# Optimization experiments

Hardware: AMD Instinct MI355X
Metric: run time of the kernel (lower is better)

Reference implementation:

```python
import jax, jax.numpy as jnp
import numpy as np

B, N, T, C, H, E = 4, 256, 36, 64, 4, 4096
D = C // H          # per-head dim
CH = 2 * C          # GAT hidden channels (embed_size * 2)


def _ln(x, g, b):
    mu = x.mean(-1, keepdims=True)
    v = ((x - mu) ** 2).mean(-1, keepdims=True)
    return (x - mu) / jnp.sqrt(v + 1e-5) * g + b


def _gat_conv(x, src, dst, W, a_s, a_d, b):
    # GATConv, heads=1, add_self_loops=False, negative_slope=0.2
    h = x @ W                                        # [N, F]
    e = jax.nn.leaky_relu((h * a_s).sum(-1)[src] + (h * a_d).sum(-1)[dst], 0.2)  # [E]
    m = jax.ops.segment_max(e, dst, num_segments=N)  # per-dst softmax (stable)
    w = jnp.exp(e - m[dst])
    s = jax.ops.segment_sum(w, dst, num_segments=N)
    alpha = w / (s[dst] + 1e-16)
    return jax.ops.segment_sum(h[src] * alpha[:, None], dst, num_segments=N) + b


def _forward(query, key, value, edge_attr, D_S, W_emb, b_emb, Wq, Wk, Wv, W_fc, b_fc,
             ln1_g, ln1_b, ln2_g, ln2_b, W_ff1, b_ff1, W_ff2, b_ff2,
             gat1_W, gat1_as, gat1_ad, gat1_b, gat2_W, gat2_as, gat2_ad, gat2_b,
             jk_W, jk_b, W_fs, b_fs, W_fg, b_fg, edge_index):
    src, dst = edge_index[0], edge_index[1]

    def gat(x):  # [N, C] -> [N, C]; 2-layer GAT with jk='max'
        h1 = jax.nn.relu(_gat_conv(x, src, dst, gat1_W, gat1_as, gat1_ad, gat1_b))
        h2 = jax.nn.relu(_gat_conv(h1, src, dst, gat2_W, gat2_as, gat2_ad, gat2_b))
        return jnp.maximum(h1, h2) @ jk_W + jk_b

    # GAT is applied to the ORIGINAL query (before D_S is added), once per timestep.
    xg = jax.vmap(jax.vmap(gat))(query.transpose(0, 2, 1, 3))  # [B, T, N, C]
    # source loop PREPENDS each timestep's output -> time axis is reversed
    X_G = xg[:, ::-1].transpose(0, 2, 1, 3)                    # [B, N, T, C]

    ds = (D_S @ W_emb + b_emb)[None, :, None, :]               # [1, N, 1, C]
    q = query + ds
    k = key + ds
    v = value + ds

    qh = q.reshape(B, N, T, H, D) @ Wq                         # per-head shared linear
    kh = k.reshape(B, N, T, H, D) @ Wk
    vh = v.reshape(B, N, T, H, D) @ Wv
    attn = jnp.einsum('bqthd,bkthd->bqkth', qh, kh)            # [B, N, N, T, H]
    # NOTE: source softmaxes over dim=1 (the QUERY axis), scaled by sqrt(embed_size)
    a = jax.nn.softmax(attn / jnp.sqrt(jnp.float32(C)), axis=1)
    o = jnp.einsum('bqkth,bkthd->bqthd', a, vh).reshape(B, N, T, C)
    o = o @ W_fc + b_fc

    M_s = _ln(o + q, ln1_g, ln1_b)                             # dropout p=0 (identity)
    ff = jax.nn.relu(M_s @ W_ff1 + b_ff1) @ W_ff2 + b_ff2
    U_s = _ln(ff + M_s, ln2_g, ln2_b)

    g = jax.nn.sigmoid(U_s @ W_fs + b_fs + X_G @ W_fg + b_fg)
    return g * U_s + (1.0 - g) * X_G


def setup_inputs():
    key = jax.random.key(0)
    ki = iter(jax.random.split(key, 64))

    def p(shape):
        fan = shape[0]
        return jax.random.normal(next(ki), shape, dtype=jnp.float32) / jnp.float32(float(np.sqrt(fan)))

    inp = {}
    inp['query'] = jax.random.normal(next(ki), (B, N, T, C), dtype=jnp.float32)
    inp['key'] = jax.random.normal(next(ki), (B, N, T, C), dtype=jnp.float32)
    inp['value'] = jax.random.normal(next(ki), (B, N, T, C), dtype=jnp.float32)
    inp['edge_attr'] = jax.random.normal(next(ki), (E,), dtype=jnp.float32)
    inp['D_S'] = jax.random.normal(next(ki), (N, N), dtype=jnp.float32)  # adj, learned param
    inp['W_emb'] = p((N, C)); inp['b_emb'] = jnp.zeros((C,), jnp.float32)
    inp['Wq'] = p((D, D)); inp['Wk'] = p((D, D)); inp['Wv'] = p((D, D))
    inp['W_fc'] = p((C, C)); inp['b_fc'] = jnp.zeros((C,), jnp.float32)
    inp['ln1_g'] = jnp.ones((C,), jnp.float32); inp['ln1_b'] = jnp.zeros((C,), jnp.float32)
    inp['ln2_g'] = jnp.ones((C,), jnp.float32); inp['ln2_b'] = jnp.zeros((C,), jnp.float32)
    inp['W_ff1'] = p((C, 4 * C)); inp['b_ff1'] = jnp.zeros((4 * C,), jnp.float32)
    inp['W_ff2'] = p((4 * C, C)); inp['b_ff2'] = jnp.zeros((C,), jnp.float32)
    inp['gat1_W'] = p((C, CH)); inp['gat1_as'] = p((CH,)); inp['gat1_ad'] = p((CH,)); inp['gat1_b'] = jnp.zeros((CH,), jnp.float32)
    inp['gat2_W'] = p((CH, CH)); inp['gat2_as'] = p((CH,)); inp['gat2_ad'] = p((CH,)); inp['gat2_b'] = jnp.zeros((CH,), jnp.float32)
    inp['jk_W'] = p((CH, C)); inp['jk_b'] = jnp.zeros((C,), jnp.float32)
    inp['W_fs'] = p((C, C)); inp['b_fs'] = jnp.zeros((C,), jnp.float32)
    inp['W_fg'] = p((C, C)); inp['b_fg'] = jnp.zeros((C,), jnp.float32)
    inp['edge_index'] = jax.random.randint(next(ki), (2, E), 0, N, dtype=jnp.int32)
    return inp


def reference(query, key, value, edge_attr, D_S, W_emb, b_emb, Wq, Wk, Wv, W_fc, b_fc,
              ln1_g, ln1_b, ln2_g, ln2_b, W_ff1, b_ff1, W_ff2, b_ff2,
              gat1_W, gat1_as, gat1_ad, gat1_b, gat2_W, gat2_as, gat2_ad, gat2_b,
              jk_W, jk_b, W_fs, b_fs, W_fg, b_fg, edge_index):
    return _forward(query, key, value, edge_attr, D_S, W_emb, b_emb, Wq, Wk, Wv, W_fc, b_fc,
                    ln1_g, ln1_b, ln2_g, ln2_b, W_ff1, b_ff1, W_ff2, b_ff2,
                    gat1_W, gat1_as, gat1_ad, gat1_b, gat2_W, gat2_as, gat2_ad, gat2_b,
                    jk_W, jk_b, W_fs, b_fs, W_fg, b_fg, edge_index)
```

## Files before the change

### kernel.cpp

```cpp
#include <hip/hip_runtime.h>

typedef unsigned short u16;
typedef unsigned int u32;

#define B_ 4
#define N_ 256
#define T_ 36
#define C_ 64
#define H_ 4
#define D_ 16
#define CH_ 128
#define E_ 4096
#define EQ_ 1408
#define G_ (B_*T_)
#define TOK_ (B_*N_*T_)

#define DS_OFF  0
#define XG_OFF  (DS_OFF + N_*C_)
#define HA_OFF  (XG_OFF + TOK_*C_)
#define HB_OFF  (HA_OFF + G_*N_*CH_/2)
#define HS_OFF  (HB_OFF + G_*N_*CH_/2)
#define HD_OFF  (HS_OFF + G_*N_)
#define INT_OFF (HD_OFF + G_*N_)
#define MS_OFF  (INT_OFF + 4608)

__device__ __forceinline__ float bf2f(u16 u){
  u32 x = ((u32)u) << 16;
  return __builtin_bit_cast(float, x);
}
__device__ __forceinline__ u16 f2bf(float f){
  u32 x = __builtin_bit_cast(u32, f);
  x += 0x7fffu + ((x >> 16) & 1u);
  return (u16)(x >> 16);
}
__device__ __forceinline__ void unpack8(uint4 u, float* f){
  f[0]=bf2f((u16)(u.x & 0xffffu)); f[1]=bf2f((u16)(u.x >> 16));
  f[2]=bf2f((u16)(u.y & 0xffffu)); f[3]=bf2f((u16)(u.y >> 16));
  f[4]=bf2f((u16)(u.z & 0xffffu)); f[5]=bf2f((u16)(u.z >> 16));
  f[6]=bf2f((u16)(u.w & 0xffffu)); f[7]=bf2f((u16)(u.w >> 16));
}
__device__ __forceinline__ uint4 pack8f(const float* f){
  uint4 u;
  u.x = (u32)f2bf(f[0]) | ((u32)f2bf(f[1]) << 16);
  u.y = (u32)f2bf(f[2]) | ((u32)f2bf(f[3]) << 16);
  u.z = (u32)f2bf(f[4]) | ((u32)f2bf(f[5]) << 16);
  u.w = (u32)f2bf(f[6]) | ((u32)f2bf(f[7]) << 16);
  return u;
}
__device__ __forceinline__ int rfl(int v){ return __builtin_amdgcn_readfirstlane(v); }

__device__ __forceinline__ void gq_from_bid(int bid, int& g, int& q){
  int xc = bid & 7, slot = bid >> 3;
  q = slot & 3;
  g = xc + ((slot >> 2) << 3);
}

#define SP_ 20
// ... 101 lines not shown
    S.c.cnt[tid] = 0;
    __syncthreads();
    for (int e = tid; e < E_; e += 256) atomicAdd(&S.c.cnt[S.c.dstL[e]], 1);
    __syncthreads();
    if (tid == 0){
      int run = 0;
      for (int i = 0; i < N_; i++){ S.c.base[i] = run; run += S.c.cnt[i]; }
      S.c.base[N_] = run;
    }
    __syncthreads();
    S.c.cnt[tid] = 0;
    __syncthreads();
    for (int e = tid; e < E_; e += 256){
      int d = S.c.dstL[e];
      int p = atomicAdd(&S.c.cnt[d], 1);
      S.c.tmp[S.c.base[d] + p] = e;
    }
    __syncthreads();
    {
      const int p0 = S.c.base[tid], p1 = S.c.base[tid] + S.c.cnt[tid];
      for (int i = p0 + 1; i < p1; i++){
        int v = S.c.tmp[i]; int j = i - 1;
        while (j >= p0 && S.c.tmp[j] > v){ S.c.tmp[j+1] = S.c.tmp[j]; j--; }
        S.c.tmp[j+1] = v;
      }
      for (int j = p0; j < p1; j++) srcs[j] = S.c.srcL[S.c.tmp[j]];
    }
    indptr[tid] = S.c.base[tid];
    if (tid == 0) indptr[N_] = S.c.base[N_];
  }
}

__global__ __launch_bounds__(256)
void k_agg1(const u16* __restrict__ hin, const float* __restrict__ hs_ws, const float* __restrict__ hd_ws,
            const int* __restrict__ indptr, const int* __restrict__ srcs,
            const float* __restrict__ bias, u16* __restrict__ hout)
{
  __shared__ int   srcs_l[EQ_];
  __shared__ float alpha_l[EQ_];
  __shared__ float hs_l[N_];
  const int bid = blockIdx.x;
  int g, q; gq_from_bid(bid, g, q);
  const int n0 = q * 64;
  const int tid = threadIdx.x;

  const int p00 = indptr[n0];
  const int pend = indptr[n0 + 64];
  const int cntE = pend - p00;
  for (int i = tid; i < cntE; i += 256) srcs_l[i] = srcs[p00 + i];
  hs_l[tid] = hs_ws[g*N_ + tid];
  __syncthreads();

  edge_softmax_par(tid, n0, indptr, p00, srcs_l, hs_l, hd_ws, g, alpha_l);
  __syncthreads();

  const int r = tid & 63;
  const int cb = rfl(tid >> 6);
  const int ch0 = cb * 32;
  const int dst = n0 + r;
  const int p0 = indptr[dst] - p00, p1 = indptr[dst+1] - p00;

  float acc[32];
  #pragma unroll
  for (int j = 0; j < 32; j++) acc[j] = 0.f;
  for (int j = p0; j < p1; j++){
    float a = alpha_l[j];
    int s = srcs_l[j];
    const uint4* hp = (const uint4*)(hin + ((size_t)(g*N_ + s))*CH_ + ch0);
    #pragma unroll
    for (int qq = 0; qq < 4; qq++){
      float hv[8]; unpack8(hp[qq], hv);
      #pragma unroll
      for (int i = 0; i < 8; i++) acc[qq*8+i] += a * hv[i];
    }
  }
  float o[32];
  #pragma unroll
  for (int j = 0; j < 32; j++){
    float v = acc[j] + bias[ch0+j];
    o[j] = v > 0.f ? v : 0.f;
  }
  u16* op = hout + ((size_t)(g*N_ + dst))*CH_ + ch0;
  #pragma unroll
  for (int j8 = 0; j8 < 32; j8 += 8)
    *(uint4*)(op + j8) = pack8f(&o[j8]);
}

__global__ __launch_bounds__(256)
void k_lin2(const u16* __restrict__ h1, const float* __restrict__ W2,
            const float* __restrict__ as2, const float* __restrict__ ad2,
            u16* __restrict__ h2, float* __restrict__ hs_ws, float* __restrict__ hd_ws)
{
  __shared__ float xs[64][129];
  __shared__ float red[2][4][64];
  const int bid = blockIdx.x;
  int g, q; gq_from_bid(bid, g, q);
  const int n0 = q * 64;
  const int tid = threadIdx.x;

  {
    #pragma unroll
    for (int it = 0; it < 4; it++){
      int idx = tid + 256*it;
      int row = idx >> 4, c8 = (idx & 15) * 8;
      uint4 u = *(const uint4*)(h1 + ((size_t)(g*N_ + n0 + row))*CH_ + c8);
      float v[8]; unpack8(u, v);
      #pragma unroll
      for (int i = 0; i < 8; i++) xs[row][c8+i] = v[i];
    }
  }
  __syncthreads();

  const int r = tid & 63;
  const int cb = rfl(tid >> 6);
  const int ch0 = cb * 32;

  float acc[32];
  #pragma unroll
  for (int j = 0; j < 32; j++) acc[j] = 0.f;
  for (int k = 0; k < 128; k++){
    float xv = xs[r][k];
    const float* wrow = W2 + k*CH_ + ch0;
    #pragma unroll
    for (int j = 0; j < 32; j++) acc[j] += xv * wrow[j];
  }
  float hs = 0.f, hd = 0.f;
  #pragma unroll
  for (int j = 0; j < 32; j++){ hs += acc[j]*as2[ch0+j]; hd += acc[j]*ad2[ch0+j]; }
  red[0][cb][r] = hs; red[1][cb][r] = hd;

  u16* hp = h2 + ((size_t)(g*N_ + n0 + r))*CH_ + ch0;
  #pragma unroll
  for (int j8 = 0; j8 < 32; j8 += 8)
    *(uint4*)(hp + j8) = pack8f(&acc[j8]);

  __syncthreads();
  if (tid < 64){
    float a = red[0][0][tid]+red[0][1][tid]+red[0][2][tid]+red[0][3][tid];
    float d = red[1][0][tid]+red[1][1][tid]+red[1][2][tid]+red[1][3][tid];
    hs_ws[g*N_ + n0 + tid] = a;
    hd_ws[g*N_ + n0 + tid] = d;
  }
}

__global__ __launch_bounds__(256)
void k_aggjk(const u16* __restrict__ h2, const float* __restrict__ hs_ws, const float* __restrict__ hd_ws,
             const int* __restrict__ indptr, const int* __restrict__ srcs,
             const float* __restrict__ b2, const u16* __restrict__ h1,
             const float* __restrict__ jkW, const float* __restrict__ jkb, float* __restrict__ xg,
             const float* __restrict__ query, const float* __restrict__ key,
             const float* __restrict__ Wq, const float* __restrict__ Wk,
             const float* __restrict__ dsb, float* __restrict__ mS)
{
  __shared__ union UJ {
    struct { int srcs_l[EQ_]; float alpha_l[EQ_]; float hs_l[N_]; } a;
    struct { u16 xs[64][136]; } l;
    struct { float qs[N_][SP_]; float wq[16][16]; float wk[16][16]; } s;
  } U;
  const int bid = blockIdx.x;
  const int tid = threadIdx.x;

  if (bid < 576){
    int g, q; gq_from_bid(bid, g, q);
    const int n0 = q * 64;
    const int b = g / T_, t = g % T_;

    const int p00 = indptr[n0];
    const int pend = indptr[n0 + 64];
    const int cntE = pend - p00;
    for (int i = tid; i < cntE; i += 256) U.a.srcs_l[i] = srcs[p00 + i];
    U.a.hs_l[tid] = hs_ws[g*N_ + tid];
    __syncthreads();

    edge_softmax_par(tid, n0, indptr, p00, U.a.srcs_l, U.a.hs_l, hd_ws, g, U.a.alpha_l);
    __syncthreads();

    const int r = tid & 63;
    const int cb = rfl(tid >> 6);
    const int ch0 = cb * 32;
    const int dst = n0 + r;
    const int p0 = indptr[dst] - p00, p1 = indptr[dst+1] - p00;

    float acc[32];
    #pragma unroll
    for (int j = 0; j < 32; j++) acc[j] = 0.f;
    for (int j = p0; j < p1; j++){
      float a = U.a.alpha_l[j];
      int s = U.a.srcs_l[j];
      const uint4* hp = (const uint4*)(h2 + ((size_t)(g*N_ + s))*CH_ + ch0);
      #pragma unroll
      for (int qq = 0; qq < 4; qq++){
        float hv[8]; unpack8(hp[qq], hv);
        #pragma unroll
        for (int i = 0; i < 8; i++) acc[qq*8+i] += a * hv[i];
      }
    }
    float o[32];
    {
      const uint4* h1p = (const uint4*)(h1 + ((size_t)(g*N_ + dst))*CH_ + ch0);
      #pragma unroll
      for (int j8 = 0; j8 < 32; j8 += 8){
        float h1v[8]; unpack8(h1p[j8>>3], h1v);
        #pragma unroll
        for (int i = 0; i < 8; i++){
          float v = acc[j8+i] + b2[ch0+j8+i];
          v = v > 0.f ? v : 0.f;
          o[j8+i] = fmaxf(h1v[i], v);
        }
      }
    }
    __syncthreads();

    #pragma unroll
    for (int j8 = 0; j8 < 32; j8 += 8)
      *(uint4*)&U.l.xs[r][ch0 + j8] = pack8f(&o[j8]);
    __syncthreads();

    const int o0 = cb * 16;
    float acc2[16];
    #pragma unroll
    for (int j = 0; j < 16; j++) acc2[j] = 0.f;
    for (int k8 = 0; k8 < 16; k8++){
      uint4 u = *(const uint4*)&U.l.xs[r][k8*8];
      float hv[8]; unpack8(u, hv);
      #pragma unroll
      for (int kk = 0; kk < 8; kk++){
        const float* wrow = jkW + (k8*8+kk)*C_ + o0;
        #pragma unroll
        for (int j = 0; j < 16; j++) acc2[j] += hv[kk] * wrow[j];
      }
    }
    float* op = xg + ((((size_t)b*N_ + n0 + r)*T_) + (T_-1-t))*C_ + o0;
    #pragma unroll
    for (int j4 = 0; j4 < 16; j4 += 4){
      float4 v = make_float4(acc2[j4]+jkb[o0+j4], acc2[j4+1]+jkb[o0+j4+1],
                             acc2[j4+2]+jkb[o0+j4+2], acc2[j4+3]+jkb[o0+j4+3]);
      *(float4*)(op + j4) = v;
    }
  } else {
    const int sb = bid - 576;
    const int b = sb / (T_*H_);
    const int rem = sb % (T_*H_);
    const int t = rem / H_;
    const int h = rem % H_;
    const int n = tid;

    U.s.wq[n>>4][n&15] = Wq[n];
    U.s.wk[n>>4][n&15] = Wk[n];

    const size_t base = ((((size_t)b*N_ + n)*T_) + t)*C_ + h*D_;
    const float* dsp = dsb + n*C_ + h*D_;

    float x[16];
    #pragma unroll
    for (int j4 = 0; j4 < 16; j4 += 4){
      float4 a = *(const float4*)(query + base + j4);
      float4 d = *(const float4*)(dsp + j4);
      x[j4]=a.x+d.x; x[j4+1]=a.y+d.y; x[j4+2]=a.z+d.z; x[j4+3]=a.w+d.w;
    }
    __syncthreads();
    #pragma unroll
    for (int j = 0; j < 16; j++){
      float a = 0.f;
      #pragma unroll
      for (int i = 0; i < 16; i++) a += x[i]*U.s.wq[i][j];
      U.s.qs[n][j] = a;
    }
    float khr[16];
    #pragma unroll
    for (int j4 = 0; j4 < 16; j4 += 4){
      float4 a = *(const float4*)(key + base + j4);
// ... 9 lines not shown
    }
    __syncthreads();

    float m[4], s[4];
    #pragma unroll
    for (int c = 0; c < 4; c++){ m[c] = -1e30f; s[c] = 0.f; }
    for (int qq = 0; qq < 64; qq++){
      #pragma unroll
      for (int c = 0; c < 4; c++){
        const float* qrow = &U.s.qs[qq + 64*c][0];
        float4 a0 = *(const float4*)(qrow);
        float4 a1 = *(const float4*)(qrow+4);
        float4 a2 = *(const float4*)(qrow+8);
        float4 a3 = *(const float4*)(qrow+12);
        float d = a0.x*khr[0]+a0.y*khr[1]+a0.z*khr[2]+a0.w*khr[3]
                + a1.x*khr[4]+a1.y*khr[5]+a1.z*khr[6]+a1.w*khr[7]
                + a2.x*khr[8]+a2.y*khr[9]+a2.z*khr[10]+a2.w*khr[11]
                + a3.x*khr[12]+a3.y*khr[13]+a3.z*khr[14]+a3.w*khr[15];
        d *= 0.125f;
        float mn = fmaxf(m[c], d);
        s[c] = s[c]*__expf(m[c]-mn) + __expf(d-mn);
        m[c] = mn;
      }
    }
    float M = fmaxf(fmaxf(m[0],m[1]), fmaxf(m[2],m[3]));
    float S = s[0]*__expf(m[0]-M) + s[1]*__expf(m[1]-M)
            + s[2]*__expf(m[2]-M) + s[3]*__expf(m[3]-M);
    mS[(size_t)sb*512 + n*2]     = M;
    mS[(size_t)sb*512 + n*2 + 1] = 1.f / S;
  }
}

__global__ __launch_bounds__(256)
void k_av(const float* __restrict__ query, const float* __restrict__ key, const float* __restrict__ value,
          const float* __restrict__ Wq, const float* __restrict__ Wk, const float* __restrict__ Wv,
          const float* __restrict__ dsb, const float* __restrict__ mS, float* __restrict__ o_ws)
{
  __shared__ float ks[N_][SP_];
  __shared__ float vs[N_][SP_];
  __shared__ float2 msl[N_];
  __shared__ float wq[16][16], wk[16][16], wv[16][16];

  const int bx = blockIdx.x;
  const int b = bx / (T_*H_);
  const int rem = bx % (T_*H_);
  const int t = rem / H_;
  const int h = rem % H_;
  const int n = threadIdx.x;

  wq[n>>4][n&15] = Wq[n];
  wk[n>>4][n&15] = Wk[n];
  wv[n>>4][n&15] = Wv[n];
  msl[n] = *(const float2*)(mS + (size_t)bx*512 + n*2);

  const size_t base = ((((size_t)b*N_ + n)*T_) + t)*C_ + h*D_;
  const float* dsp = dsb + n*C_ + h*D_;

  float ds16[16];
  #pragma unroll
  for (int j4 = 0; j4 < 16; j4 += 4){
    float4 d = *(const float4*)(dsp + j4);
    ds16[j4]=d.x; ds16[j4+1]=d.y; ds16[j4+2]=d.z; ds16[j4+3]=d.w;
  }
  __syncthreads();

  float x[16];
  #pragma unroll
  for (int j4 = 0; j4 < 16; j4 += 4){
    float4 a = *(const float4*)(key + base + j4);
    x[j4]=a.x+ds16[j4]; x[j4+1]=a.y+ds16[j4+1]; x[j4+2]=a.z+ds16[j4+2]; x[j4+3]=a.w+ds16[j4+3];
  }
  #pragma unroll
  for (int j = 0; j < 16; j++){
    float a = 0.f;
    #pragma unroll
    for (int i = 0; i < 16; i++) a += x[i]*wk[i][j];
    ks[n][j] = a;
  }
  #pragma unroll
  for (int j4 = 0; j4 < 16; j4 += 4){
    float4 a = *(const float4*)(value + base + j4);
    x[j4]=a.x+ds16[j4]; x[j4+1]=a.y+ds16[j4+1]; x[j4+2]=a.z+ds16[j4+2]; x[j4+3]=a.w+ds16[j4+3];
  }
  #pragma unroll
  for (int j = 0; j < 16; j++){
    float a = 0.f;
    #pragma unroll
    for (int i = 0; i < 16; i++) a += x[i]*wv[i][j];
    vs[n][j] = a;
  }
  float qhr[16];
  #pragma unroll
  for (int j4 = 0; j4 < 16; j4 += 4){
    float4 a = *(const float4*)(query + base + j4);
    x[j4]=a.x+ds16[j4]; x[j4+1]=a.y+ds16[j4+1]; x[j4+2]=a.z+ds16[j4+2]; x[j4+3]=a.w+ds16[j4+3];
  }
  #pragma unroll
  for (int j = 0; j < 16; j++){
    float a = 0.f;
    #pragma unroll
    for (int i = 0; i < 16; i++) a += x[i]*wq[i][j];
    qhr[j] = a;
  }
  __syncthreads();

  float o0[16], o1[16];
  #pragma unroll
  for (int j = 0; j < 16; j++){ o0[j] = 0.f; o1[j] = 0.f; }
  for (int k = 0; k < N_; k += 2){
    {
      const float* krow = &ks[k][0];
      float4 a0 = *(const float4*)(krow);
      float4 a1 = *(const float4*)(krow+4);
      float4 a2 = *(const float4*)(krow+8);
      float4 a3 = *(const float4*)(krow+12);
      float d = a0.x*qhr[0]+a0.y*qhr[1]+a0.z*qhr[2]+a0.w*qhr[3]
              + a1.x*qhr[4]+a1.y*qhr[5]+a1.z*qhr[6]+a1.w*qhr[7]
              + a2.x*qhr[8]+a2.y*qhr[9]+a2.z*qhr[10]+a2.w*qhr[11]
              + a3.x*qhr[12]+a3.y*qhr[13]+a3.z*qhr[14]+a3.w*qhr[15];
      float2 ms0 = msl[k];
      float p = __expf(d*0.125f - ms0.x) * ms0.y;
      const float* vrow = &vs[k][0];
      float4 v0 = *(const float4*)(vrow);
      float4 v1 = *(const float4*)(vrow+4);
      float4 v2 = *(const float4*)(vrow+8);
      float4 v3 = *(const float4*)(vrow+12);
      o0[0]+=p*v0.x; o0[1]+=p*v0.y; o0[2]+=p*v0.z; o0[3]+=p*v0.w;
      o0[4]+=p*v1.x; o0[5]+=p*v1.y; o0[6]+=p*v1.z; o0[7]+=p*v1.w;
      o0[8]+=p*v2.x; o0[9]+=p*v2.y; o0[10]+=p*v2.z; o0[11]+=p*v2.w;
      o0[12]+=p*v3.x; o0[13]+=p*v3.y; o0[14]+=p*v3.z; o0[15]+=p*v3.w;
    }
    {
      const float* krow = &ks[k+1][0];
      float4 a0 = *(const float4*)(krow);
      float4 a1 = *(const float4*)(krow+4);
      float4 a2 = *(const float4*)(krow+8);
      float4 a3 = *(const float4*)(krow+12);
      float d = a0.x*qhr[0]+a0.y*qhr[1]+a0.z*qhr[2]+a0.w*qhr[3]
              + a1.x*qhr[4]+a1.y*qhr[5]+a1.z*qhr[6]+a1.w*qhr[7]
              + a2.x*qhr[8]+a2.y*qhr[9]+a2.z*qhr[10]+a2.w*qhr[11]
              + a3.x*qhr[12]+a3.y*qhr[13]+a3.z*qhr[14]+a3.w*qhr[15];
      float2 ms1 = msl[k+1];
      float p = __expf(d*0.125f - ms1.x) * ms1.y;
      const float* vrow = &vs[k+1][0];
      float4 v0 = *(const float4*)(vrow);
      float4 v1 = *(const float4*)(vrow+4);
      float4 v2 = *(const float4*)(vrow+8);
      float4 v3 = *(const float4*)(vrow+12);
      o1[0]+=p*v0.x; o1[1]+=p*v0.y; o1[2]+=p*v0.z; o1[3]+=p*v0.w;
      o1[4]+=p*v1.x; o1[5]+=p*v1.y; o1[6]+=p*v1.z; o1[7]+=p*v1.w;
      o1[8]+=p*v2.x; o1[9]+=p*v2.y; o1[10]+=p*v2.z; o1[11]+=p*v2.w;
      o1[12]+=p*v3.x; o1[13]+=p*v3.y; o1[14]+=p*v3.z; o1[15]+=p*v3.w;
    }
  }
  float* op = o_ws + base;
  #pragma unroll
  for (int j4 = 0; j4 < 16; j4 += 4)
    *(float4*)(op + j4) = make_float4(o0[j4]+o1[j4], o0[j4+1]+o1[j4+1],
                                      o0[j4+2]+o1[j4+2], o0[j4+3]+o1[j4+3]);
}

__global__ __launch_bounds__(256)
void k_final(const float* __restrict__ query, const float* __restrict__ dsb,
             const float* __restrict__ o_ws, const float* __restrict__ xg_ws,
             const float* __restrict__ Wfc, const float* __restrict__ bfc,
             const float* __restrict__ ln1g, const float* __restrict__ ln1b,
             const float* __restrict__ ln2g, const float* __restrict__ ln2b,
             const float* __restrict__ Wff1, const float* __restrict__ bff1,
             const float* __restrict__ Wff2, const float* __restrict__ bff2,
             const float* __restrict__ Wfs, const float* __restrict__ bfs,
             const float* __restrict__ Wfg, const float* __restrict__ bfg,
             float* __restrict__ out)
{
  __shared__ u16 smA[64*66];
  __shared__ u16 smB[64*66];
  __shared__ union UH { u16 h[128*66]; float o[64*66]; } HH;
  __shared__ float lnxA[4][64];
  __shared__ float lnxB[4][64];

  const int tid = threadIdx.x;
  const int token0 = blockIdx.x * 64;
  const int w = rfl(tid >> 6);
  const int tok = tid & 63;
  const int c0 = w * 16;

  #pragma unroll
  for (int it = 0; it < 4; it++){
    int idx = tid + 256*it;
    int tk = idx >> 4, c4 = (idx & 15) * 4;
    int gtok = token0 + tk;
    int n = (gtok / T_) & (N_-1);
    float4 ov = *(const float4*)(o_ws + (size_t)gtok*C_ + c4);
// ... 118 lines not shown
    float xv = bf2f(HH.h[i*66 + tok]);
    const float* wsr = Wfs + i*C_ + c0;
    const float* wgr = Wfg + i*C_ + c0;
    #pragma unroll
    for (int j = 0; j < 16; j++) ga[j] += uv*wsr[j] + xv*wgr[j];
  }
  float res[16];
  #pragma unroll
  for (int j = 0; j < 16; j++){
    float a = ga[j] + bfs[c0+j] + bfg[c0+j];
    float gg = 1.f / (1.f + __expf(-a));
    float xgv = bf2f(HH.h[(c0+j)*66 + tok]);
    res[j] = gg*us[j] + (1.f-gg)*xgv;
  }
  __syncthreads();
  #pragma unroll
  for (int j = 0; j < 16; j++) HH.o[(c0+j)*66 + tok] = res[j];
  __syncthreads();
  #pragma unroll
  for (int it = 0; it < 4; it++){
    int idx = tid + 256*it;
    int tk = idx >> 4, c4 = (idx & 15) * 4;
    int gtok = token0 + tk;
    float4 v = make_float4(HH.o[(c4+0)*66+tk], HH.o[(c4+1)*66+tk],
                           HH.o[(c4+2)*66+tk], HH.o[(c4+3)*66+tk]);
    *(float4*)(out + (size_t)gtok*C_ + c4) = v;
  }
}

extern "C" void kernel_launch(void* const* d_in, const int* in_sizes, int n_in,
                              void* d_out, int out_size, void* d_ws, size_t ws_size,
                              hipStream_t stream)
{
  (void)in_sizes; (void)n_in; (void)out_size; (void)ws_size;
  const float* query = (const float*)d_in[0];
  const float* key   = (const float*)d_in[1];
  const float* value = (const float*)d_in[2];
  const float* DSm   = (const float*)d_in[4];
  const float* Wemb  = (const float*)d_in[5];
  const float* bemb  = (const float*)d_in[6];
  const float* Wq    = (const float*)d_in[7];
  const float* Wk    = (const float*)d_in[8];
  const float* Wv    = (const float*)d_in[9];
  const float* Wfc   = (const float*)d_in[10];
  const float* bfc   = (const float*)d_in[11];
  const float* ln1g  = (const float*)d_in[12];
  const float* ln1b  = (const float*)d_in[13];
  const float* ln2g  = (const float*)d_in[14];
  const float* ln2b  = (const float*)d_in[15];
  const float* Wff1  = (const float*)d_in[16];
  const float* bff1  = (const float*)d_in[17];
  const float* Wff2  = (const float*)d_in[18];
  const float* bff2  = (const float*)d_in[19];
  const float* g1W   = (const float*)d_in[20];
  const float* g1as  = (const float*)d_in[21];
  const float* g1ad  = (const float*)d_in[22];
  const float* g1b   = (const float*)d_in[23];
  const float* g2W   = (const float*)d_in[24];
  const float* g2as  = (const float*)d_in[25];
  const float* g2ad  = (const float*)d_in[26];
  const float* g2b   = (const float*)d_in[27];
  const float* jkW   = (const float*)d_in[28];
  const float* jkb   = (const float*)d_in[29];
  const float* Wfs   = (const float*)d_in[30];
  const float* bfs   = (const float*)d_in[31];
  const float* Wfg   = (const float*)d_in[32];
  const float* bfg   = (const float*)d_in[33];
  const int* ei      = (const int*)d_in[34];
  float* out = (float*)d_out;

  float* wf     = (float*)d_ws;
  float* dsb    = wf + DS_OFF;
  float* xg_ws  = wf + XG_OFF;
  u16*   hA     = (u16*)(wf + HA_OFF);
  u16*   hB     = (u16*)(wf + HB_OFF);
  float* o_ws   = wf + HA_OFF;
  float* hs_ws  = wf + HS_OFF;
  float* hd_ws  = wf + HD_OFF;
  int*   indptr = (int*)(wf + INT_OFF);
  int*   srcs   = indptr + 260;
  float* mS     = wf + MS_OFF;

  k_pre  <<<dim3(641),  dim3(256), 0, stream>>>(query, g1W, g1as, g1ad, hA, hs_ws, hd_ws,
                                                DSm, Wemb, bemb, dsb, ei, indptr, srcs);
  k_agg1 <<<dim3(576),  dim3(256), 0, stream>>>(hA, hs_ws, hd_ws, indptr, srcs, g1b, hB);
  k_lin2 <<<dim3(576),  dim3(256), 0, stream>>>(hB, g2W, g2as, g2ad, hA, hs_ws, hd_ws);
  k_aggjk<<<dim3(1152), dim3(256), 0, stream>>>(hA, hs_ws, hd_ws, indptr, srcs, g2b, hB,
                                                jkW, jkb, xg_ws,
                                                query, key, Wq, Wk, dsb, mS);
  k_av   <<<dim3(576),  dim3(256), 0, stream>>>(query, key, value, Wq, Wk, Wv, dsb, mS, o_ws);
  k_final<<<dim3(576),  dim3(256), 0, stream>>>(query, dsb, o_ws, xg_ws,
      Wfc, bfc, ln1g, ln1b, ln2g, ln2b,
      Wff1, bff1, Wff2, bff2,
      Wfs, bfs, Wfg, bfg, out);
}
```

Before: 304.6 us.

## Rebalance kernel pairing: attention stats with GAT layer 1, AV with GAT layer 2

The attention softmax-statistics blocks move from the layer-2 aggregation kernel into the layer-1 aggregation kernel. The attention AV blocks are merged into the layer-2 aggregation plus JK kernel, which removes one launch and lets independent work share the GPU. To run AV at the same time as aggregation, the AV output gets its own workspace region rather than aliasing the hA buffer. If the workspace is too small, the code falls back to two sequential launches. The cost is a larger shared-memory union and larger workspace use.

```diff
diff --git a/kernel.cpp b/kernel.cpp
--- a/kernel.cpp
+++ b/kernel.cpp
@@ -23,6 +23,7 @@
 #define HD_OFF  (HS_OFF + G_*N_)
 #define INT_OFF (HD_OFF + G_*N_)
 #define MS_OFF  (INT_OFF + 4608)
+#define O_SEP_OFF (MS_OFF + 576*512)
 
 __device__ __forceinline__ float bf2f(u16 u){
   u32 x = ((u32)u) << 16;
@@ -190,129 +191,15 @@
 }
 
 __global__ __launch_bounds__(256)
-void k_agg1(const u16* __restrict__ hin, const float* __restrict__ hs_ws, const float* __restrict__ hd_ws,
-            const int* __restrict__ indptr, const int* __restrict__ srcs,
-            const float* __restrict__ bias, u16* __restrict__ hout)
+void k_agg1stat(const u16* __restrict__ hin, const float* __restrict__ hs_ws, const float* __restrict__ hd_ws,
+                const int* __restrict__ indptr, const int* __restrict__ srcs,
+                const float* __restrict__ bias, u16* __restrict__ hout,
+                const float* __restrict__ query, const float* __restrict__ key,
+                const float* __restrict__ Wq, const float* __restrict__ Wk,
+                const float* __restrict__ dsb, float* __restrict__ mS)
 {
-  __shared__ int   srcs_l[EQ_];
-  __shared__ float alpha_l[EQ_];
-  __shared__ float hs_l[N_];
-  const int bid = blockIdx.x;
-  int g, q; gq_from_bid(bid, g, q);
-  const int n0 = q * 64;
-  const int tid = threadIdx.x;
-
-  const int p00 = indptr[n0];
-  const int pend = indptr[n0 + 64];
-  const int cntE = pend - p00;
-  for (int i = tid; i < cntE; i += 256) srcs_l[i] = srcs[p00 + i];
-  hs_l[tid] = hs_ws[g*N_ + tid];
-  __syncthreads();
-
-  edge_softmax_par(tid, n0, indptr, p00, srcs_l, hs_l, hd_ws, g, alpha_l);
-  __syncthreads();
-
-  const int r = tid & 63;
-  const int cb = rfl(tid >> 6);
-  const int ch0 = cb * 32;
-  const int dst = n0 + r;
-  const int p0 = indptr[dst] - p00, p1 = indptr[dst+1] - p00;
-
-  float acc[32];
-  #pragma unroll
-  for (int j = 0; j < 32; j++) acc[j] = 0.f;
-  for (int j = p0; j < p1; j++){
-    float a = alpha_l[j];
-    int s = srcs_l[j];
-    const uint4* hp = (const uint4*)(hin + ((size_t)(g*N_ + s))*CH_ + ch0);
-    #pragma unroll
-    for (int qq = 0; qq < 4; qq++){
-      float hv[8]; unpack8(hp[qq], hv);
-      #pragma unroll
-      for (int i = 0; i < 8; i++) acc[qq*8+i] += a * hv[i];
-    }
-  }
-  float o[32];
-  #pragma unroll
-  for (int j = 0; j < 32; j++){
-    float v = acc[j] + bias[ch0+j];
-    o[j] = v > 0.f ? v : 0.f;
-  }
-  u16* op = hout + ((size_t)(g*N_ + dst))*CH_ + ch0;
-  #pragma unroll
-  for (int j8 = 0; j8 < 32; j8 += 8)
-    *(uint4*)(op + j8) = pack8f(&o[j8]);
-}
-
-__global__ __launch_bounds__(256)
-void k_lin2(const u16* __restrict__ h1, const float* __restrict__ W2,
-            const float* __restrict__ as2, const float* __restrict__ ad2,
-            u16* __restrict__ h2, float* __restrict__ hs_ws, float* __restrict__ hd_ws)
-{
-  __shared__ float xs[64][129];
-  __shared__ float red[2][4][64];
-  const int bid = blockIdx.x;
-  int g, q; gq_from_bid(bid, g, q);
-  const int n0 = q * 64;
-  const int tid = threadIdx.x;
-
-  {
-    #pragma unroll
-    for (int it = 0; it < 4; it++){
-      int idx = tid + 256*it;
-      int row = idx >> 4, c8 = (idx & 15) * 8;
-      uint4 u = *(const uint4*)(h1 + ((size_t)(g*N_ + n0 + row))*CH_ + c8);
-      float v[8]; unpack8(u, v);
-      #pragma unroll
-      for (int i = 0; i < 8; i++) xs[row][c8+i] = v[i];
-    }
-  }
-  __syncthreads();
-
-  const int r = tid & 63;
-  const int cb = rfl(tid >> 6);
-  const int ch0 = cb * 32;
-
-  float acc[32];
-  #pragma unroll
-  for (int j = 0; j < 32; j++) acc[j] = 0.f;
-  for (int k = 0; k < 128; k++){
-    float xv = xs[r][k];
-    const float* wrow = W2 + k*CH_ + ch0;
-    #pragma unroll
-    for (int j = 0; j < 32; j++) acc[j] += xv * wrow[j];
-  }
-  float hs = 0.f, hd = 0.f;
-  #pragma unroll
-  for (int j = 0; j < 32; j++){ hs += acc[j]*as2[ch0+j]; hd += acc[j]*ad2[ch0+j]; }
-  red[0][cb][r] = hs; red[1][cb][r] = hd;
-
-  u16* hp = h2 + ((size_t)(g*N_ + n0 + r))*CH_ + ch0;
-  #pragma unroll
-  for (int j8 = 0; j8 < 32; j8 += 8)
-    *(uint4*)(hp + j8) = pack8f(&acc[j8]);
-
-  __syncthreads();
-  if (tid < 64){
-    float a = red[0][0][tid]+red[0][1][tid]+red[0][2][tid]+red[0][3][tid];
-    float d = red[1][0][tid]+red[1][1][tid]+red[1][2][tid]+red[1][3][tid];
-    hs_ws[g*N_ + n0 + tid] = a;
-    hd_ws[g*N_ + n0 + tid] = d;
-  }
-}
-
-__global__ __launch_bounds__(256)
-void k_aggjk(const u16* __restrict__ h2, const float* __restrict__ hs_ws, const float* __restrict__ hd_ws,
-             const int* __restrict__ indptr, const int* __restrict__ srcs,
-             const float* __restrict__ b2, const u16* __restrict__ h1,
-             const float* __restrict__ jkW, const float* __restrict__ jkb, float* __restrict__ xg,
-             const float* __restrict__ query, const float* __restrict__ key,
-             const float* __restrict__ Wq, const float* __restrict__ Wk,
-             const float* __restrict__ dsb, float* __restrict__ mS)
-{
-  __shared__ union UJ {
+  __shared__ union UA {
     struct { int srcs_l[EQ_]; float alpha_l[EQ_]; float hs_l[N_]; } a;
-    struct { u16 xs[64][136]; } l;
     struct { float qs[N_][SP_]; float wq[16][16]; float wk[16][16]; } s;
   } U;
   const int bid = blockIdx.x;
@@ -321,7 +208,6 @@
   if (bid < 576){
     int g, q; gq_from_bid(bid, g, q);
     const int n0 = q * 64;
-    const int b = g / T_, t = g % T_;
 
     const int p00 = indptr[n0];
     const int pend = indptr[n0 + 64];
@@ -345,7 +231,7 @@
     for (int j = p0; j < p1; j++){
       float a = U.a.alpha_l[j];
       int s = U.a.srcs_l[j];
-      const uint4* hp = (const uint4*)(h2 + ((size_t)(g*N_ + s))*CH_ + ch0);
+      const uint4* hp = (const uint4*)(hin + ((size_t)(g*N_ + s))*CH_ + ch0);
       #pragma unroll
       for (int qq = 0; qq < 4; qq++){
         float hv[8]; unpack8(hp[qq], hv);
@@ -354,47 +240,15 @@
       }
     }
     float o[32];
-    {
-      const uint4* h1p = (const uint4*)(h1 + ((size_t)(g*N_ + dst))*CH_ + ch0);
-      #pragma unroll
-      for (int j8 = 0; j8 < 32; j8 += 8){
-        float h1v[8]; unpack8(h1p[j8>>3], h1v);
-        #pragma unroll
-        for (int i = 0; i < 8; i++){
-          float v = acc[j8+i] + b2[ch0+j8+i];
-          v = v > 0.f ? v : 0.f;
-          o[j8+i] = fmaxf(h1v[i], v);
-        }
-      }
-    }
-    __syncthreads();
-
+    #pragma unroll
+    for (int j = 0; j < 32; j++){
+      float v = acc[j] + bias[ch0+j];
+      o[j] = v > 0.f ? v : 0.f;
+    }
+    u16* op = hout + ((size_t)(g*N_ + dst))*CH_ + ch0;
     #pragma unroll
     for (int j8 = 0; j8 < 32; j8 += 8)
-      *(uint4*)&U.l.xs[r][ch0 + j8] = pack8f(&o[j8]);
-    __syncthreads();
-
-    const int o0 = cb * 16;
-    float acc2[16];
-    #pragma unroll
-    for (int j = 0; j < 16; j++) acc2[j] = 0.f;
-    for (int k8 = 0; k8 < 16; k8++){
-      uint4 u = *(const uint4*)&U.l.xs[r][k8*8];
-      float hv[8]; unpack8(u, hv);
-      #pragma unroll
-      for (int kk = 0; kk < 8; kk++){
-        const float* wrow = jkW + (k8*8+kk)*C_ + o0;
-        #pragma unroll
-        for (int j = 0; j < 16; j++) acc2[j] += hv[kk] * wrow[j];
-      }
-    }
-    float* op = xg + ((((size_t)b*N_ + n0 + r)*T_) + (T_-1-t))*C_ + o0;
-    #pragma unroll
-    for (int j4 = 0; j4 < 16; j4 += 4){
-      float4 v = make_float4(acc2[j4]+jkb[o0+j4], acc2[j4+1]+jkb[o0+j4+1],
-                             acc2[j4+2]+jkb[o0+j4+2], acc2[j4+3]+jkb[o0+j4+3]);
-      *(float4*)(op + j4) = v;
-    }
+      *(uint4*)(op + j8) = pack8f(&o[j8]);
   } else {
     const int sb = bid - 576;
     const int b = sb / (T_*H_);
@@ -470,132 +324,277 @@
 }
 
 __global__ __launch_bounds__(256)
-void k_av(const float* __restrict__ query, const float* __restrict__ key, const float* __restrict__ value,
-          const float* __restrict__ Wq, const float* __restrict__ Wk, const float* __restrict__ Wv,
-          const float* __restrict__ dsb, const float* __restrict__ mS, float* __restrict__ o_ws)
+void k_lin2(const u16* __restrict__ h1, const float* __restrict__ W2,
+            const float* __restrict__ as2, const float* __restrict__ ad2,
+            u16* __restrict__ h2, float* __restrict__ hs_ws, float* __restrict__ hd_ws)
 {
-  __shared__ float ks[N_][SP_];
-  __shared__ float vs[N_][SP_];
-  __shared__ float2 msl[N_];
-  __shared__ float wq[16][16], wk[16][16], wv[16][16];
-
-  const int bx = blockIdx.x;
-  const int b = bx / (T_*H_);
-  const int rem = bx % (T_*H_);
-  const int t = rem / H_;
-  const int h = rem % H_;
-  const int n = threadIdx.x;
-
-  wq[n>>4][n&15] = Wq[n];
-  wk[n>>4][n&15] = Wk[n];
-  wv[n>>4][n&15] = Wv[n];
-  msl[n] = *(const float2*)(mS + (size_t)bx*512 + n*2);
-
-  const size_t base = ((((size_t)b*N_ + n)*T_) + t)*C_ + h*D_;
-  const float* dsp = dsb + n*C_ + h*D_;
-
-  float ds16[16];
-  #pragma unroll
-  for (int j4 = 0; j4 < 16; j4 += 4){
-    float4 d = *(const float4*)(dsp + j4);
-    ds16[j4]=d.x; ds16[j4+1]=d.y; ds16[j4+2]=d.z; ds16[j4+3]=d.w;
-  }
-  __syncthreads();
-
-  float x[16];
-  #pragma unroll
-  for (int j4 = 0; j4 < 16; j4 += 4){
-    float4 a = *(const float4*)(key + base + j4);
-    x[j4]=a.x+ds16[j4]; x[j4+1]=a.y+ds16[j4+1]; x[j4+2]=a.z+ds16[j4+2]; x[j4+3]=a.w+ds16[j4+3];
-  }
-  #pragma unroll
-  for (int j = 0; j < 16; j++){
-    float a = 0.f;
-    #pragma unroll
-    for (int i = 0; i < 16; i++) a += x[i]*wk[i][j];
-    ks[n][j] = a;
-  }
-  #pragma unroll
-  for (int j4 = 0; j4 < 16; j4 += 4){
-    float4 a = *(const float4*)(value + base + j4);
-    x[j4]=a.x+ds16[j4]; x[j4+1]=a.y+ds16[j4+1]; x[j4+2]=a.z+ds16[j4+2]; x[j4+3]=a.w+ds16[j4+3];
-  }
-  #pragma unroll
-  for (int j = 0; j < 16; j++){
-    float a = 0.f;
-    #pragma unroll
-    for (int i = 0; i < 16; i++) a += x[i]*wv[i][j];
-    vs[n][j] = a;
-  }
-  float qhr[16];
-  #pragma unroll
-  for (int j4 = 0; j4 < 16; j4 += 4){
-    float4 a = *(const float4*)(query + base + j4);
-    x[j4]=a.x+ds16[j4]; x[j4+1]=a.y+ds16[j4+1]; x[j4+2]=a.z+ds16[j4+2]; x[j4+3]=a.w+ds16[j4+3];
-  }
-  #pragma unroll
-  for (int j = 0; j < 16; j++){
-    float a = 0.f;
-    #pragma unroll
-    for (int i = 0; i < 16; i++) a += x[i]*wq[i][j];
-    qhr[j] = a;
-  }
-  __syncthreads();
-
-  float o0[16], o1[16];
-  #pragma unroll
-  for (int j = 0; j < 16; j++){ o0[j] = 0.f; o1[j] = 0.f; }
-  for (int k = 0; k < N_; k += 2){
+  __shared__ float xs[64][129];
+  __shared__ float red[2][4][64];
+  const int bid = blockIdx.x;
+  int g, q; gq_from_bid(bid, g, q);
+  const int n0 = q * 64;
+  const int tid = threadIdx.x;
+
+  {
+    #pragma unroll
+    for (int it = 0; it < 4; it++){
+      int idx = tid + 256*it;
+      int row = idx >> 4, c8 = (idx & 15) * 8;
+      uint4 u = *(const uint4*)(h1 + ((size_t)(g*N_ + n0 + row))*CH_ + c8);
+      float v[8]; unpack8(u, v);
+      #pragma unroll
+      for (int i = 0; i < 8; i++) xs[row][c8+i] = v[i];
+    }
+  }
+  __syncthreads();
+
+  const int r = tid & 63;
+  const int cb = rfl(tid >> 6);
+  const int ch0 = cb * 32;
+
+  float acc[32];
+  #pragma unroll
+  for (int j = 0; j < 32; j++) acc[j] = 0.f;
+  for (int k = 0; k < 128; k++){
+    float xv = xs[r][k];
+    const float* wrow = W2 + k*CH_ + ch0;
+    #pragma unroll
+    for (int j = 0; j < 32; j++) acc[j] += xv * wrow[j];
+  }
+  float hs = 0.f, hd = 0.f;
+  #pragma unroll
+  for (int j = 0; j < 32; j++){ hs += acc[j]*as2[ch0+j]; hd += acc[j]*ad2[ch0+j]; }
+  red[0][cb][r] = hs; red[1][cb][r] = hd;
+
+  u16* hp = h2 + ((size_t)(g*N_ + n0 + r))*CH_ + ch0;
+  #pragma unroll
+  for (int j8 = 0; j8 < 32; j8 += 8)
+    *(uint4*)(hp + j8) = pack8f(&acc[j8]);
+
+  __syncthreads();
+  if (tid < 64){
+    float a = red[0][0][tid]+red[0][1][tid]+red[0][2][tid]+red[0][3][tid];
+    float d = red[1][0][tid]+red[1][1][tid]+red[1][2][tid]+red[1][3][tid];
+    hs_ws[g*N_ + n0 + tid] = a;
+    hd_ws[g*N_ + n0 + tid] = d;
+  }
+}
+
+__global__ __launch_bounds__(256)
+void k_agg2av(const u16* __restrict__ h2, const float* __restrict__ hs_ws, const float* __restrict__ hd_ws,
+              const int* __restrict__ indptr, const int* __restrict__ srcs,
+              const float* __restrict__ b2, const u16* __restrict__ h1,
+              const float* __restrict__ jkW, const float* __restrict__ jkb, float* __restrict__ xg,
+              const float* __restrict__ query, const float* __restrict__ key, const float* __restrict__ value,
+              const float* __restrict__ Wq, const float* __restrict__ Wk, const float* __restrict__ Wv,
+              const float* __restrict__ dsb, const float* __restrict__ mS, float* __restrict__ o_ws,
+              int bid_base)
+{
+  __shared__ union UJ {
+    struct { int srcs_l[EQ_]; float alpha_l[EQ_]; float hs_l[N_]; } a;
+    struct { u16 xs[64][136]; } l;
+    struct { float ks[N_][SP_]; float vs[N_][SP_]; float2 msl[N_];
+             float wq[16][16]; float wk[16][16]; float wv[16][16]; } v;
+  } U;
+  const int bid = blockIdx.x + bid_base;
+  const int tid = threadIdx.x;
+
+  if (bid < 576){
+    int g, q; gq_from_bid(bid, g, q);
+    const int n0 = q * 64;
+    const int b = g / T_, t = g % T_;
+
+    const int p00 = indptr[n0];
+    const int pend = indptr[n0 + 64];
+    const int cntE = pend - p00;
+    for (int i = tid; i < cntE; i += 256) U.a.srcs_l[i] = srcs[p00 + i];
+    U.a.hs_l[tid] = hs_ws[g*N_ + tid];
+    __syncthreads();
+
+    edge_softmax_par(tid, n0, indptr, p00, U.a.srcs_l, U.a.hs_l, hd_ws, g, U.a.alpha_l);
+    __syncthreads();
+
+    const int r = tid & 63;
+    const int cb = rfl(tid >> 6);
+    const int ch0 = cb * 32;
+    const int dst = n0 + r;
+    const int p0 = indptr[dst] - p00, p1 = indptr[dst+1] - p00;
+
+    float acc[32];
+    #pragma unroll
+    for (int j = 0; j < 32; j++) acc[j] = 0.f;
+    for (int j = p0; j < p1; j++){
+      float a = U.a.alpha_l[j];
+      int s = U.a.srcs_l[j];
+      const uint4* hp = (const uint4*)(h2 + ((size_t)(g*N_ + s))*CH_ + ch0);
+      #pragma unroll
+      for (int qq = 0; qq < 4; qq++){
+        float hv[8]; unpack8(hp[qq], hv);
+        #pragma unroll
+        for (int i = 0; i < 8; i++) acc[qq*8+i] += a * hv[i];
+      }
+    }
+    float o[32];
     {
-      const float* krow = &ks[k][0];
-      float4 a0 = *(const float4*)(krow);
-      float4 a1 = *(const float4*)(krow+4);
-      float4 a2 = *(const float4*)(krow+8);
-      float4 a3 = *(const float4*)(krow+12);
-      float d = a0.x*qhr[0]+a0.y*qhr[1]+a0.z*qhr[2]+a0.w*qhr[3]
-              + a1.x*qhr[4]+a1.y*qhr[5]+a1.z*qhr[6]+a1.w*qhr[7]
-              + a2.x*qhr[8]+a2.y*qhr[9]+a2.z*qhr[10]+a2.w*qhr[11]
-              + a3.x*qhr[12]+a3.y*qhr[13]+a3.z*qhr[14]+a3.w*qhr[15];
-      float2 ms0 = msl[k];
-      float p = __expf(d*0.125f - ms0.x) * ms0.y;
-      const float* vrow = &vs[k][0];
-      float4 v0 = *(const float4*)(vrow);
-      float4 v1 = *(const float4*)(vrow+4);
-      float4 v2 = *(const float4*)(vrow+8);
-      float4 v3 = *(const float4*)(vrow+12);
-      o0[0]+=p*v0.x; o0[1]+=p*v0.y; o0[2]+=p*v0.z; o0[3]+=p*v0.w;
-      o0[4]+=p*v1.x; o0[5]+=p*v1.y; o0[6]+=p*v1.z; o0[7]+=p*v1.w;
-      o0[8]+=p*v2.x; o0[9]+=p*v2.y; o0[10]+=p*v2.z; o0[11]+=p*v2.w;
-      o0[12]+=p*v3.x; o0[13]+=p*v3.y; o0[14]+=p*v3.z; o0[15]+=p*v3.w;
-    }
-    {
-      const float* krow = &ks[k+1][0];
-      float4 a0 = *(const float4*)(krow);
-      float4 a1 = *(const float4*)(krow+4);
-      float4 a2 = *(const float4*)(krow+8);
-      float4 a3 = *(const float4*)(krow+12);
-      float d = a0.x*qhr[0]+a0.y*qhr[1]+a0.z*qhr[2]+a0.w*qhr[3]
-              + a1.x*qhr[4]+a1.y*qhr[5]+a1.z*qhr[6]+a1.w*qhr[7]
-              + a2.x*qhr[8]+a2.y*qhr[9]+a2.z*qhr[10]+a2.w*qhr[11]
-              + a3.x*qhr[12]+a3.y*qhr[13]+a3.z*qhr[14]+a3.w*qhr[15];
-      float2 ms1 = msl[k+1];
-      float p = __expf(d*0.125f - ms1.x) * ms1.y;
-      const float* vrow = &vs[k+1][0];
-      float4 v0 = *(const float4*)(vrow);
-      float4 v1 = *(const float4*)(vrow+4);
-      float4 v2 = *(const float4*)(vrow+8);
-      float4 v3 = *(const float4*)(vrow+12);
-      o1[0]+=p*v0.x; o1[1]+=p*v0.y; o1[2]+=p*v0.z; o1[3]+=p*v0.w;
-      o1[4]+=p*v1.x; o1[5]+=p*v1.y; o1[6]+=p*v1.z; o1[7]+=p*v1.w;
-      o1[8]+=p*v2.x; o1[9]+=p*v2.y; o1[10]+=p*v2.z; o1[11]+=p*v2.w;
-      o1[12]+=p*v3.x; o1[13]+=p*v3.y; o1[14]+=p*v3.z; o1[15]+=p*v3.w;
-    }
-  }
-  float* op = o_ws + base;
-  #pragma unroll
-  for (int j4 = 0; j4 < 16; j4 += 4)
-    *(float4*)(op + j4) = make_float4(o0[j4]+o1[j4], o0[j4+1]+o1[j4+1],
-                                      o0[j4+2]+o1[j4+2], o0[j4+3]+o1[j4+3]);
+      const uint4* h1p = (const uint4*)(h1 + ((size_t)(g*N_ + dst))*CH_ + ch0);
+      #pragma unroll
+      for (int j8 = 0; j8 < 32; j8 += 8){
+        float h1v[8]; unpack8(h1p[j8>>3], h1v);
+        #pragma unroll
+        for (int i = 0; i < 8; i++){
+          float v = acc[j8+i] + b2[ch0+j8+i];
+          v = v > 0.f ? v : 0.f;
+          o[j8+i] = fmaxf(h1v[i], v);
+        }
+      }
+    }
+    __syncthreads();
+
+    #pragma unroll
+    for (int j8 = 0; j8 < 32; j8 += 8)
+      *(uint4*)&U.l.xs[r][ch0 + j8] = pack8f(&o[j8]);
+    __syncthreads();
+
+    const int o0 = cb * 16;
+    float acc2[16];
+    #pragma unroll
+    for (int j = 0; j < 16; j++) acc2[j] = 0.f;
+    for (int k8 = 0; k8 < 16; k8++){
+      uint4 u = *(const uint4*)&U.l.xs[r][k8*8];
+      float hv[8]; unpack8(u, hv);
+      #pragma unroll
+      for (int kk = 0; kk < 8; kk++){
+        const float* wrow = jkW + (k8*8+kk)*C_ + o0;
+        #pragma unroll
+        for (int j = 0; j < 16; j++) acc2[j] += hv[kk] * wrow[j];
+      }
+    }
+    float* op = xg + ((((size_t)b*N_ + n0 + r)*T_) + (T_-1-t))*C_ + o0;
+    #pragma unroll
+    for (int j4 = 0; j4 < 16; j4 += 4){
+      float4 v = make_float4(acc2[j4]+jkb[o0+j4], acc2[j4+1]+jkb[o0+j4+1],
+                             acc2[j4+2]+jkb[o0+j4+2], acc2[j4+3]+jkb[o0+j4+3]);
+      *(float4*)(op + j4) = v;
+    }
+  } else {
+    const int sb = bid - 576;
+    const int b = sb / (T_*H_);
+    const int rem = sb % (T_*H_);
+    const int t = rem / H_;
+    const int h = rem % H_;
+    const int n = tid;
+
+    U.v.wq[n>>4][n&15] = Wq[n];
+    U.v.wk[n>>4][n&15] = Wk[n];
+    U.v.wv[n>>4][n&15] = Wv[n];
+    U.v.msl[n] = *(const float2*)(mS + (size_t)sb*512 + n*2);
+
+    const size_t base = ((((size_t)b*N_ + n)*T_) + t)*C_ + h*D_;
+    const float* dsp = dsb + n*C_ + h*D_;
+
+    float ds16[16];
+    #pragma unroll
+    for (int j4 = 0; j4 < 16; j4 += 4){
+      float4 d = *(const float4*)(dsp + j4);
+      ds16[j4]=d.x; ds16[j4+1]=d.y; ds16[j4+2]=d.z; ds16[j4+3]=d.w;
+    }
+    __syncthreads();
+
+    float x[16];
+    #pragma unroll
+    for (int j4 = 0; j4 < 16; j4 += 4){
+      float4 a = *(const float4*)(key + base + j4);
+      x[j4]=a.x+ds16[j4]; x[j4+1]=a.y+ds16[j4+1]; x[j4+2]=a.z+ds16[j4+2]; x[j4+3]=a.w+ds16[j4+3];
+    }
+    #pragma unroll
+    for (int j = 0; j < 16; j++){
+      float a = 0.f;
+      #pragma unroll
+      for (int i = 0; i < 16; i++) a += x[i]*U.v.wk[i][j];
+      U.v.ks[n][j] = a;
+    }
+    #pragma unroll
+    for (int j4 = 0; j4 < 16; j4 += 4){
+      float4 a = *(const float4*)(value + base + j4);
+      x[j4]=a.x+ds16[j4]; x[j4+1]=a.y+ds16[j4+1]; x[j4+2]=a.z+ds16[j4+2]; x[j4+3]=a.w+ds16[j4+3];
+    }
+    #pragma unroll
+    for (int j = 0; j < 16; j++){
+      float a = 0.f;
+      #pragma unroll
+      for (int i = 0; i < 16; i++) a += x[i]*U.v.wv[i][j];
+      U.v.vs[n][j] = a;
+    }
+    float qhr[16];
+    #pragma unroll
+    for (int j4 = 0; j4 < 16; j4 += 4){
+      float4 a = *(const float4*)(query + base + j4);
+      x[j4]=a.x+ds16[j4]; x[j4+1]=a.y+ds16[j4+1]; x[j4+2]=a.z+ds16[j4+2]; x[j4+3]=a.w+ds16[j4+3];
+    }
+    #pragma unroll
+    for (int j = 0; j < 16; j++){
+      float a = 0.f;
+      #pragma unroll
+      for (int i = 0; i < 16; i++) a += x[i]*U.v.wq[i][j];
+      qhr[j] = a;
+    }
+    __syncthreads();
+
+    float o0[16], o1[16];
+    #pragma unroll
+    for (int j = 0; j < 16; j++){ o0[j] = 0.f; o1[j] = 0.f; }
+    for (int k = 0; k < N_; k += 2){
+      {
+        const float* krow = &U.v.ks[k][0];
+        float4 a0 = *(const float4*)(krow);
+        float4 a1 = *(const float4*)(krow+4);
+        float4 a2 = *(const float4*)(krow+8);
+        float4 a3 = *(const float4*)(krow+12);
+        float d = a0.x*qhr[0]+a0.y*qhr[1]+a0.z*qhr[2]+a0.w*qhr[3]
+                + a1.x*qhr[4]+a1.y*qhr[5]+a1.z*qhr[6]+a1.w*qhr[7]
+                + a2.x*qhr[8]+a2.y*qhr[9]+a2.z*qhr[10]+a2.w*qhr[11]
+                + a3.x*qhr[12]+a3.y*qhr[13]+a3.z*qhr[14]+a3.w*qhr[15];
+        float2 ms0 = U.v.msl[k];
+        float p = __expf(d*0.125f - ms0.x) * ms0.y;
+        const float* vrow = &U.v.vs[k][0];
+        float4 v0 = *(const float4*)(vrow);
+        float4 v1 = *(const float4*)(vrow+4);
+        float4 v2 = *(const float4*)(vrow+8);
+        float4 v3 = *(const float4*)(vrow+12);
+        o0[0]+=p*v0.x; o0[1]+=p*v0.y; o0[2]+=p*v0.z; o0[3]+=p*v0.w;
+        o0[4]+=p*v1.x; o0[5]+=p*v1.y; o0[6]+=p*v1.z; o0[7]+=p*v1.w;
+        o0[8]+=p*v2.x; o0[9]+=p*v2.y; o0[10]+=p*v2.z; o0[11]+=p*v2.w;
+        o0[12]+=p*v3.x; o0[13]+=p*v3.y; o0[14]+=p*v3.z; o0[15]+=p*v3.w;
+      }
+      {
+        const float* krow = &U.v.ks[k+1][0];
+        float4 a0 = *(const float4*)(krow);
+        float4 a1 = *(const float4*)(krow+4);
+        float4 a2 = *(const float4*)(krow+8);
+        float4 a3 = *(const float4*)(krow+12);
+        float d = a0.x*qhr[0]+a0.y*qhr[1]+a0.z*qhr[2]+a0.w*qhr[3]
+                + a1.x*qhr[4]+a1.y*qhr[5]+a1.z*qhr[6]+a1.w*qhr[7]
+                + a2.x*qhr[8]+a2.y*qhr[9]+a2.z*qhr[10]+a2.w*qhr[11]
+                + a3.x*qhr[12]+a3.y*qhr[13]+a3.z*qhr[14]+a3.w*qhr[15];
+        float2 ms1 = U.v.msl[k+1];
+        float p = __expf(d*0.125f - ms1.x) * ms1.y;
+        const float* vrow = &U.v.vs[k+1][0];
+        float4 v0 = *(const float4*)(vrow);
+        float4 v1 = *(const float4*)(vrow+4);
+        float4 v2 = *(const float4*)(vrow+8);
+        float4 v3 = *(const float4*)(vrow+12);
+        o1[0]+=p*v0.x; o1[1]+=p*v0.y; o1[2]+=p*v0.z; o1[3]+=p*v0.w;
+        o1[4]+=p*v1.x; o1[5]+=p*v1.y; o1[6]+=p*v1.z; o1[7]+=p*v1.w;
+        o1[8]+=p*v2.x; o1[9]+=p*v2.y; o1[10]+=p*v2.z; o1[11]+=p*v2.w;
+        o1[12]+=p*v3.x; o1[13]+=p*v3.y; o1[14]+=p*v3.z; o1[15]+=p*v3.w;
+      }
+    }
+    float* op = o_ws + base;
+    #pragma unroll
+    for (int j4 = 0; j4 < 16; j4 += 4)
+      *(float4*)(op + j4) = make_float4(o0[j4]+o1[j4], o0[j4+1]+o1[j4+1],
+                                        o0[j4+2]+o1[j4+2], o0[j4+3]+o1[j4+3]);
+  }
 }
 
 __global__ __launch_bounds__(256)
@@ -780,7 +779,7 @@
                               void* d_out, int out_size, void* d_ws, size_t ws_size,
                               hipStream_t stream)
 {
-  (void)in_sizes; (void)n_in; (void)out_size; (void)ws_size;
+  (void)in_sizes; (void)n_in; (void)out_size;
   const float* query = (const float*)d_in[0];
   const float* key   = (const float*)d_in[1];
   const float* value = (const float*)d_in[2];
@@ -822,22 +821,34 @@
   float* xg_ws  = wf + XG_OFF;
   u16*   hA     = (u16*)(wf + HA_OFF);
   u16*   hB     = (u16*)(wf + HB_OFF);
-  float* o_ws   = wf + HA_OFF;
   float* hs_ws  = wf + HS_OFF;
   float* hd_ws  = wf + HD_OFF;
   int*   indptr = (int*)(wf + INT_OFF);
   int*   srcs   = indptr + 260;
   float* mS     = wf + MS_OFF;
 
-  k_pre  <<<dim3(641),  dim3(256), 0, stream>>>(query, g1W, g1as, g1ad, hA, hs_ws, hd_ws,
-                                                DSm, Wemb, bemb, dsb, ei, indptr, srcs);
-  k_agg1 <<<dim3(576),  dim3(256), 0, stream>>>(hA, hs_ws, hd_ws, indptr, srcs, g1b, hB);
-  k_lin2 <<<dim3(576),  dim3(256), 0, stream>>>(hB, g2W, g2as, g2ad, hA, hs_ws, hd_ws);
-  k_aggjk<<<dim3(1152), dim3(256), 0, stream>>>(hA, hs_ws, hd_ws, indptr, srcs, g2b, hB,
-                                                jkW, jkb, xg_ws,
-                                                query, key, Wq, Wk, dsb, mS);
-  k_av   <<<dim3(576),  dim3(256), 0, stream>>>(query, key, value, Wq, Wk, Wv, dsb, mS, o_ws);
-  k_final<<<dim3(576),  dim3(256), 0, stream>>>(query, dsb, o_ws, xg_ws,
+  const size_t need = (size_t)(O_SEP_OFF + TOK_*C_) * 4;
+  const bool sep = ws_size >= need;
+  float* o_ws = sep ? (wf + O_SEP_OFF) : (wf + HA_OFF);
+
+  k_pre     <<<dim3(641),  dim3(256), 0, stream>>>(query, g1W, g1as, g1ad, hA, hs_ws, hd_ws,
+                                                   DSm, Wemb, bemb, dsb, ei, indptr, srcs);
+  k_agg1stat<<<dim3(1152), dim3(256), 0, stream>>>(hA, hs_ws, hd_ws, indptr, srcs, g1b, hB,
+                                                   query, key, Wq, Wk, dsb, mS);
+  k_lin2    <<<dim3(576),  dim3(256), 0, stream>>>(hB, g2W, g2as, g2ad, hA, hs_ws, hd_ws);
+  if (sep){
+    k_agg2av<<<dim3(1152), dim3(256), 0, stream>>>(hA, hs_ws, hd_ws, indptr, srcs, g2b, hB,
+                                                   jkW, jkb, xg_ws,
+                                                   query, key, value, Wq, Wk, Wv, dsb, mS, o_ws, 0);
+  } else {
+    k_agg2av<<<dim3(576),  dim3(256), 0, stream>>>(hA, hs_ws, hd_ws, indptr, srcs, g2b, hB,
+                                                   jkW, jkb, xg_ws,
+                                                   query, key, value, Wq, Wk, Wv, dsb, mS, o_ws, 0);
+    k_agg2av<<<dim3(576),  dim3(256), 0, stream>>>(hA, hs_ws, hd_ws, indptr, srcs, g2b, hB,
+                                                   jkW, jkb, xg_ws,
+                                                   query, key, value, Wq, Wk, Wv, dsb, mS, o_ws, 576);
+  }
+  k_final   <<<dim3(576),  dim3(256), 0, stream>>>(query, dsb, o_ws, xg_ws,
       Wfc, bfc, ln1g, ln1b, ln2g, ln2b,
       Wff1, bff1, Wff2, bff2,
       Wfs, bfs, Wfg, bfg, out);
```

Result: faster. 280.0 us, median of 3 (-8.1%).
